# Kernel optimization log

Hardware: AMD Instinct MI355X
Metric: run time of the kernel (lower is better)

Reference implementation:

```python
import jax, jax.numpy as jnp
import numpy as np

N = 50000          # nodes
E = 1_600_000      # edges (avg degree 32)
IN_N, IN_E = 16, 1 # fc_encoder hardwired input dims
H = 128            # per-layer out_node/out_edge channels (out//2 = 64 inner)
BN_EPS = 1e-5


def setup_inputs() -> dict:
    key = jax.random.key(0)
    ks = jax.random.split(key, 32)
    d = {}
    d["x"] = jax.random.normal(ks[0], (N, IN_N), jnp.float32)
    d["edge_attr"] = jax.random.normal(ks[1], (E, IN_E), jnp.float32)
    d["edge_index"] = jax.random.randint(ks[2], (2, E), 0, N)
    i = 3
    for l, (ni, ei) in enumerate([(IN_N, IN_E), (H, H)]):
        s_n = 1.0 / np.sqrt(ni)
        s_e = 1.0 / np.sqrt(ei)
        s_h = 1.0 / np.sqrt(H)
        d[f"l{l}_Wn"] = jax.random.normal(ks[i], (H // 2, ni), jnp.float32) * s_n; i += 1
        d[f"l{l}_We"] = jax.random.normal(ks[i], (H // 2, ei), jnp.float32) * s_e; i += 1
        d[f"l{l}_Wfn"] = jax.random.normal(ks[i], (H, H), jnp.float32) * s_h; i += 1
        d[f"l{l}_bfn"] = jax.random.normal(ks[i], (H,), jnp.float32) * s_h; i += 1
        d[f"l{l}_Wfe"] = jax.random.normal(ks[i], (H, H), jnp.float32) * s_h; i += 1
        d[f"l{l}_bfe"] = jax.random.normal(ks[i], (H,), jnp.float32) * s_h; i += 1
        d[f"l{l}_g"] = jax.random.uniform(ks[i], (H,), jnp.float32, 0.5, 1.5); i += 1
        d[f"l{l}_b"] = jax.random.normal(ks[i], (H,), jnp.float32) * 0.1; i += 1
        d[f"l{l}_rm"] = jax.random.normal(ks[i], (H,), jnp.float32) * 0.1; i += 1
        d[f"l{l}_rv"] = jax.random.uniform(ks[i], (H,), jnp.float32, 0.5, 1.5); i += 1
    return d


def _layer(x, ea, src, dst, Wn, We, Wfn, bfn, Wfe, bfe, g, b, rm, rv):
    # NodeEdgeInteraction_node (eval mode: dropout = identity)
    n1 = jax.nn.relu(x @ Wn.T)            # [N, H/2]
    e1 = jax.nn.relu(ea @ We.T)           # [E, H/2]
    # edge_updater: cat([n1[src] + n1[dst], e1])
    e2 = jnp.concatenate([n1[src] + n1[dst], e1], axis=-1)      # [E, H]
    # propagate: message = e1, sum-aggregate at destination (edge_index[1])
    agg = jax.ops.segment_sum(e1, dst, num_segments=x.shape[0])  # [N, H/2]
    n2 = jnp.concatenate([agg, n1], axis=-1)                     # [N, H]
    n2 = jax.nn.relu(n2 @ Wfn.T + bfn)
    e2 = jax.nn.relu(e2 @ Wfe.T + bfe)
    # BatchNorm1d (eval: running stats)
    n2 = (n2 - rm) * jax.lax.rsqrt(rv + BN_EPS) * g + b
    return n2, e2


def reference(x, edge_attr, edge_index,
              l0_Wn, l0_We, l0_Wfn, l0_bfn, l0_Wfe, l0_bfe, l0_g, l0_b, l0_rm, l0_rv,
              l1_Wn, l1_We, l1_Wfn, l1_bfn, l1_Wfe, l1_bfe, l1_g, l1_b, l1_rm, l1_rv):
    src, dst = edge_index[0], edge_index[1]
    x, edge_attr = _layer(x, edge_attr, src, dst,
                          l0_Wn, l0_We, l0_Wfn, l0_bfn, l0_Wfe, l0_bfe,
                          l0_g, l0_b, l0_rm, l0_rv)
    x, edge_attr = _layer(x, edge_attr, src, dst,
                          l1_Wn, l1_We, l1_Wfn, l1_bfn, l1_Wfe, l1_bfe,
                          l1_g, l1_b, l1_rm, l1_rv)
    return x  # GNNEncoder returns node embeddings only
```

## Files before the change

kernel.cpp:

```cpp
#include <hip/hip_runtime.h>

typedef unsigned short u16;
typedef __attribute__((ext_vector_type(8))) short short8;
typedef __attribute__((ext_vector_type(4))) float floatx4;

#define NN 50000
#define NE 1600000
#define BN_EPS 1e-5f

__device__ __forceinline__ float bfu(u16 u) {
    union { unsigned u32; float f; } v; v.u32 = ((unsigned)u) << 16; return v.f;
}
__device__ __forceinline__ u16 f2bf(float f) {
    union { float f; unsigned u; } v; v.f = f;
    unsigned r = v.u + 0x7FFFu + ((v.u >> 16) & 1u);
    return (u16)(r >> 16);
}
__device__ __forceinline__ float ldf(const void* p, int i, int m) {
    return m ? ((const float*)p)[i] : bfu(((const u16*)p)[i]);
}

__global__ __launch_bounds__(256) void k_detect(const u16* __restrict__ x, int* __restrict__ mode) {
    float mx = 0.f;
    for (int i = threadIdx.x; i < 4096; i += 256) mx = fmaxf(mx, fabsf(bfu(x[i])));
#pragma unroll
    for (int o = 32; o > 0; o >>= 1) mx = fmaxf(mx, __shfl_down(mx, o));
    __shared__ float s[4];
    if ((threadIdx.x & 63) == 0) s[threadIdx.x >> 6] = mx;
    __syncthreads();
    if (threadIdx.x == 0) {
        float m2 = fmaxf(fmaxf(s[0], s[1]), fmaxf(s[2], s[3]));
        mode[0] = (m2 > 1e4f) ? 1 : 0;
    }
}

__global__ __launch_bounds__(256) void k_cvtw(const void* __restrict__ W0, const void* __restrict__ W1,
                                              const void* __restrict__ W2, const void* __restrict__ W3,
                                              const void* __restrict__ W4,
                                              u16* __restrict__ dst, const int* __restrict__ mf) {
    int m = mf[0];
    int i = blockIdx.x * 256 + threadIdx.x;
    const void* src; int off;
    if (i < 16384)      { src = W0; off = i; }
    else if (i < 24576) { src = W1; off = i - 16384; }
    else if (i < 40960) { src = W2; off = i - 24576; }
    else if (i < 49152) { src = W3; off = i - 40960; }
    else                { src = W4; off = i - 49152; }
    dst[i] = m ? f2bf(((const float*)src)[off]) : ((const u16*)src)[off];
}

__global__ __launch_bounds__(256) void k_enc0(const void* __restrict__ x, const void* __restrict__ Wn,
                                              u16* __restrict__ n1, const int* __restrict__ mf) {
    int m = mf[0];
    __shared__ float Wns[64 * 17];
    __shared__ float xsh[4][16];
    int t = threadIdx.x;
    int n0 = blockIdx.x * 4;
    for (int i = t; i < 1024; i += 256) Wns[(i >> 4) * 17 + (i & 15)] = ldf(Wn, i, m);
    if (t < 64) xsh[t >> 4][t & 15] = ldf(x, n0 * 16 + t, m);
    __syncthreads();
    int n = t >> 6, c = t & 63;
    float acc = 0.f;
#pragma unroll
    for (int i = 0; i < 16; i++) acc += xsh[n][i] * Wns[c * 17 + i];
    n1[(n0 + n) * 64 + c] = f2bf(fmaxf(acc, 0.f));
}

__global__ __launch_bounds__(256) void k_esum(const void* __restrict__ ea, const int* __restrict__ ei,
                                              float* __restrict__ sp, float* __restrict__ sn,
                                              const int* __restrict__ mf) {
    int m = mf[0];
    int e = blockIdx.x * 256 + threadIdx.x;
    float a = ldf(ea, e, m);
    int d = ei[NE + e];
    if (a > 0.f) atomicAdd(sp + d, a);
    else if (a < 0.f) atomicAdd(sn + d, a);
}

__global__ void k_pn(const void* __restrict__ We0, const void* __restrict__ Wfe0,
                     float* __restrict__ PN, const int* __restrict__ mf) {
    int m = mf[0];
    int j = threadIdx.x;
    float p = 0.f, n = 0.f;
    for (int k = 0; k < 64; k++) {
        float w = ldf(We0, k, m);
        float wf = ldf(Wfe0, j * 128 + 64 + k, m);
        p += fmaxf(w, 0.f) * wf;
        n += fminf(w, 0.f) * wf;
    }
    PN[j] = p; PN[128 + j] = n;
}

__global__ __launch_bounds__(256) void k_node_l0(
    const u16* __restrict__ n1l0, const float* __restrict__ sp, const float* __restrict__ sn,
    const void* __restrict__ We0, const u16* __restrict__ Wfn0c, const void* __restrict__ bfn0,
    const void* __restrict__ g0, const void* __restrict__ b0,
    const void* __restrict__ rm0, const void* __restrict__ rv0,
    const u16* __restrict__ Wn1c, u16* __restrict__ n1l1, const int* __restrict__ mf) {
    int m = mf[0];
    __shared__ __align__(16) u16 fs[64][136];
    __shared__ __align__(16) u16 xs[64][136];
    int t = threadIdx.x;
    int n0 = blockIdx.x * 64;
    {
        int col = t & 127;
        int rbase = t >> 7;
        float wp = 0.f, wn = 0.f;
        if (col < 64) { float w0 = ldf(We0, col, m); wp = fmaxf(w0, 0.f); wn = fminf(w0, 0.f); }
#pragma unroll
        for (int i = 0; i < 32; i++) {
            int row = rbase + 2 * i;
            int n = n0 + row;
            float v = 0.f;
            if (n < NN) v = (col < 64) ? (wp * sp[n] + wn * sn[n]) : bfu(n1l0[n * 64 + col - 64]);
            fs[row][col] = f2bf(v);
        }
    }
    __syncthreads();
    int lane = t & 63, w = t >> 6, q = lane >> 4, nidx = lane & 15;
    {
        const u16* ar = &fs[w * 16 + nidx][0];
        short8 a0 = *(const short8*)&ar[q * 8];
        short8 a1 = *(const short8*)&ar[32 + q * 8];
        short8 a2 = *(const short8*)&ar[64 + q * 8];
        short8 a3 = *(const short8*)&ar[96 + q * 8];
#pragma unroll
        for (int jt = 0; jt < 8; jt++) {
            int j = jt * 16 + nidx;
            const u16* wr = Wfn0c + j * 128;
            floatx4 acc = {0.f, 0.f, 0.f, 0.f};
            acc = __builtin_amdgcn_mfma_f32_16x16x32_bf16(a0, *(const short8*)&wr[q * 8], acc, 0, 0, 0);
            acc = __builtin_amdgcn_mfma_f32_16x16x32_bf16(a1, *(const short8*)&wr[32 + q * 8], acc, 0, 0, 0);
            acc = __builtin_amdgcn_mfma_f32_16x16x32_bf16(a2, *(const short8*)&wr[64 + q * 8], acc, 0, 0, 0);
            acc = __builtin_amdgcn_mfma_f32_16x16x32_bf16(a3, *(const short8*)&wr[96 + q * 8], acc, 0, 0, 0);
            float bias = ldf(bfn0, j, m);
            float sc = ldf(g0, j, m) * rsqrtf(ldf(rv0, j, m) + BN_EPS);
            float sh = ldf(b0, j, m) - ldf(rm0, j, m) * sc;
#pragma unroll
            for (int r = 0; r < 4; r++) {
                int row = w * 16 + q * 4 + r;
                xs[row][j] = f2bf(fmaxf(acc[r] + bias, 0.f) * sc + sh);
            }
        }
    }
    __syncthreads();
    {
        const u16* ar = &xs[w * 16 + nidx][0];
        short8 a0 = *(const short8*)&ar[q * 8];
        short8 a1 = *(const short8*)&ar[32 + q * 8];
        short8 a2 = *(const short8*)&ar[64 + q * 8];
        short8 a3 = *(const short8*)&ar[96 + q * 8];
#pragma unroll
        for (int jt = 0; jt < 4; jt++) {
            int j = jt * 16 + nidx;
            const u16* wr = Wn1c + j * 128;
            floatx4 acc = {0.f, 0.f, 0.f, 0.f};
            acc = __builtin_amdgcn_mfma_f32_16x16x32_bf16(a0, *(const short8*)&wr[q * 8], acc, 0, 0, 0);
            acc = __builtin_amdgcn_mfma_f32_16x16x32_bf16(a1, *(const short8*)&wr[32 + q * 8], acc, 0, 0, 0);
            acc = __builtin_amdgcn_mfma_f32_16x16x32_bf16(a2, *(const short8*)&wr[64 + q * 8], acc, 0, 0, 0);
            acc = __builtin_amdgcn_mfma_f32_16x16x32_bf16(a3, *(const short8*)&wr[96 + q * 8], acc, 0, 0, 0);
#pragma unroll
            for (int r = 0; r < 4; r++) {
                int row = w * 16 + q * 4 + r;
                int n = n0 + row;
                if (n < NN) n1l1[n * 64 + j] = f2bf(fmaxf(acc[r], 0.f));
            }
        }
    }
}

__global__ __launch_bounds__(256) void k_edge(
    const void* __restrict__ ea, const int* __restrict__ ei,
    const u16* __restrict__ n1l0,
    const u16* __restrict__ Wfe0c, const void* __restrict__ bfe0,
    const float* __restrict__ PN,
    const u16* __restrict__ We1c,
    float* __restrict__ agg, const int* __restrict__ mf) {
    int m = mf[0];
    __shared__ __align__(16) u16 h0s[16][72];
    __shared__ __align__(16) u16 h1s[16][136];
    __shared__ float aes[16];
    __shared__ int dsts[16];
    __shared__ int srcs[16];
    int t = threadIdx.x;
    int e0 = blockIdx.x * 16;
    if (t < 16) {
        int eg = e0 + t;
        aes[t] = ldf(ea, eg, m);
        srcs[t] = ei[eg];
        dsts[t] = ei[NE + eg];
    }
    __syncthreads();
#pragma unroll
    for (int i = 0; i < 4; i++) {
        int idx = t + i * 256;
        int e = idx >> 6, c = idx & 63;
        float v = bfu(n1l0[srcs[e] * 64 + c]) + bfu(n1l0[dsts[e] * 64 + c]);
        h0s[e][c] = f2bf(v);
    }
    __syncthreads();
    int lane = t & 63;
    int w = t >> 6;
    int q = lane >> 4;
    int nidx = lane & 15;
    short8 a0 = *(const short8*)&h0s[nidx][q * 8];
    short8 a1 = *(const short8*)&h0s[nidx][32 + q * 8];
#pragma unroll
    for (int jj = 0; jj < 2; jj++) {
        int jt = 2 * w + jj;
        int j = jt * 16 + nidx;
        const u16* wrow = Wfe0c + j * 128;
        short8 b0 = *(const short8*)&wrow[q * 8];
        short8 b1 = *(const short8*)&wrow[32 + q * 8];
        floatx4 acc = {0.f, 0.f, 0.f, 0.f};
        acc = __builtin_amdgcn_mfma_f32_16x16x32_bf16(a0, b0, acc, 0, 0, 0);
        acc = __builtin_amdgcn_mfma_f32_16x16x32_bf16(a1, b1, acc, 0, 0, 0);
        float bias = ldf(bfe0, j, m);
        float Pj = PN[j], Nj = PN[128 + j];
#pragma unroll
        for (int r = 0; r < 4; r++) {
            int e = q * 4 + r;
            float a = aes[e];
            float v = acc[r] + bias + a * (a > 0.f ? Pj : Nj);
            h1s[e][j] = f2bf(fmaxf(v, 0.f));
        }
    }
    __syncthreads();
    {
        int c = w * 16 + nidx;
        const u16* wrow = We1c + c * 128;
        floatx4 acc = {0.f, 0.f, 0.f, 0.f};
#pragma unroll
        for (int ks = 0; ks < 4; ks++) {
            short8 aa = *(const short8*)&h1s[nidx][ks * 32 + q * 8];
            short8 bb = *(const short8*)&wrow[ks * 32 + q * 8];
            acc = __builtin_amdgcn_mfma_f32_16x16x32_bf16(aa, bb, acc, 0, 0, 0);
        }
#pragma unroll
        for (int r = 0; r < 4; r++) {
            int e = q * 4 + r;
            float v = fmaxf(acc[r], 0.f);
            atomicAdd(agg + dsts[e] * 64 + c, v);
        }
    }
}

__global__ __launch_bounds__(256) void k_node_l1(
    const u16* __restrict__ n1l1, const float* __restrict__ agg,
    const u16* __restrict__ Wfn1c, const void* __restrict__ bfn1,
    const void* __restrict__ g1, const void* __restrict__ b1,
    const void* __restrict__ rm1, const void* __restrict__ rv1,
    void* __restrict__ out, const int* __restrict__ mf) {
    int m = mf[0];
    __shared__ __align__(16) u16 fs[64][136];
    int t = threadIdx.x;
    int n0 = blockIdx.x * 64;
    {
        int col = t & 127;
        int rbase = t >> 7;
#pragma unroll
        for (int i = 0; i < 32; i++) {
            int row = rbase + 2 * i;
            int n = n0 + row;
            float v = 0.f;
            if (n < NN) v = (col < 64) ? agg[n * 64 + col] : bfu(n1l1[n * 64 + col - 64]);
            fs[row][col] = f2bf(v);
        }
    }
    __syncthreads();
    int lane = t & 63, w = t >> 6, q = lane >> 4, nidx = lane & 15;
    const u16* ar = &fs[w * 16 + nidx][0];
    short8 a0 = *(const short8*)&ar[q * 8];
    short8 a1 = *(const short8*)&ar[32 + q * 8];
    short8 a2 = *(const short8*)&ar[64 + q * 8];
    short8 a3 = *(const short8*)&ar[96 + q * 8];
#pragma unroll
    for (int jt = 0; jt < 8; jt++) {
        int j = jt * 16 + nidx;
        const u16* wr = Wfn1c + j * 128;
        floatx4 acc = {0.f, 0.f, 0.f, 0.f};
        acc = __builtin_amdgcn_mfma_f32_16x16x32_bf16(a0, *(const short8*)&wr[q * 8], acc, 0, 0, 0);
        acc = __builtin_amdgcn_mfma_f32_16x16x32_bf16(a1, *(const short8*)&wr[32 + q * 8], acc, 0, 0, 0);
        acc = __builtin_amdgcn_mfma_f32_16x16x32_bf16(a2, *(const short8*)&wr[64 + q * 8], acc, 0, 0, 0);
        acc = __builtin_amdgcn_mfma_f32_16x16x32_bf16(a3, *(const short8*)&wr[96 + q * 8], acc, 0, 0, 0);
        float bias = ldf(bfn1, j, m);
        float sc = ldf(g1, j, m) * rsqrtf(ldf(rv1, j, m) + BN_EPS);
        float sh = ldf(b1, j, m) - ldf(rm1, j, m) * sc;
#pragma unroll
        for (int r = 0; r < 4; r++) {
            int row = w * 16 + q * 4 + r;
            int n = n0 + row;
            if (n < NN) {
                float v = fmaxf(acc[r] + bias, 0.f) * sc + sh;
                if (m) ((float*)out)[n * 128 + j] = v;
                else   ((u16*)out)[n * 128 + j] = f2bf(v);
            }
        }
    }
}

extern "C" void kernel_launch(void* const* d_in, const int* in_sizes, int n_in,
                              void* d_out, int out_size, void* d_ws, size_t ws_size,
                              hipStream_t stream) {
    const void* x    = d_in[0];
    const void* ea   = d_in[1];
    const int*  ei   = (const int*)d_in[2];
    const void* Wn0  = d_in[3];
    const void* We0  = d_in[4];
    const void* Wfn0 = d_in[5];
    const void* bfn0 = d_in[6];
    const void* Wfe0 = d_in[7];
    const void* bfe0 = d_in[8];
    const void* g0   = d_in[9];
    const void* b0   = d_in[10];
    const void* rm0  = d_in[11];
    const void* rv0  = d_in[12];
    const void* Wn1  = d_in[13];
    const void* We1  = d_in[14];
    const void* Wfn1 = d_in[15];
    const void* bfn1 = d_in[16];
    const void* g1   = d_in[19];
    const void* b1   = d_in[20];
    const void* rm1  = d_in[21];
    const void* rv1  = d_in[22];

    float* wsf   = (float*)d_ws;
    float* agg   = wsf;
    u16*   n1l0  = (u16*)(wsf + 3200000);
    u16*   n1l1  = (u16*)(wsf + 4800000);
    float* sp    = wsf + 6400000;
    float* sn    = wsf + 6450000;
    float* PN    = wsf + 6500000;
    u16*   Wc    = (u16*)(wsf + 6500256);
    int*   mode  = (int*)(wsf + 6533024);
    u16* Wfe0c = Wc;
    u16* We1c  = Wc + 16384;
    u16* Wfn0c = Wc + 24576;
    u16* Wn1c  = Wc + 40960;
    u16* Wfn1c = Wc + 49152;

    hipMemsetAsync(sp, 0, 100000 * sizeof(float), stream);
    hipMemsetAsync(agg, 0, 3200000 * sizeof(float), stream);

    k_detect<<<1, 256, 0, stream>>>((const u16*)x, mode);
    k_cvtw<<<256, 256, 0, stream>>>(Wfe0, We1, Wfn0, Wn1, Wfn1, Wc, mode);
    k_enc0<<<12500, 256, 0, stream>>>(x, Wn0, n1l0, mode);
    k_esum<<<6250, 256, 0, stream>>>(ea, ei, sp, sn, mode);
    k_pn<<<1, 128, 0, stream>>>(We0, Wfe0, PN, mode);
    k_node_l0<<<782, 256, 0, stream>>>(n1l0, sp, sn, We0, Wfn0c, bfn0,
                                       g0, b0, rm0, rv0, Wn1c, n1l1, mode);
    k_edge<<<100000, 256, 0, stream>>>(ea, ei, n1l0, Wfe0c, bfe0, PN, We1c, agg, mode);
    k_node_l1<<<782, 256, 0, stream>>>(n1l1, agg, Wfn1c, bfn1,
                                       g1, b1, rm1, rv1, d_out, mode);
}
```

Before: 713.6 us.

## Sort edges by destination (CSR) and aggregate per-node in shared memory

Builds a destination-sorted CSR by counting in-degree, running a three-kernel prefix scan, and scattering the source index plus edge attribute into permuted arrays. The edge kernel then handles blocks of 8 destination nodes: it caches their n1 rows in shared memory and accumulates messages with shared-memory atomics, so the 1.6M×64 global atomicAdds and the agg memset go away. The cost is extra scan and scatter passes with global atomics, and partially filled 16-edge tiles. The packing into perm assumes source indices fit in 16 bits, which fails for N=50000 (src up to 49999 > 65535? no, fits), though block work is now imbalanced across nodes of differing degree.

After: 1.129 ms. 58.2% more time.

```diff
diff --git a/kernel.cpp b/kernel.cpp
--- a/kernel.cpp
+++ b/kernel.cpp
@@ -7,6 +7,8 @@
 #define NN 50000
 #define NE 1600000
 #define BN_EPS 1e-5f
+#define NPB 8
+#define NSCAN 196
 
 __device__ __forceinline__ float bfu(u16 u) {
     union { unsigned u32; float f; } v; v.u32 = ((unsigned)u) << 16; return v.f;
@@ -68,13 +70,72 @@
 
 __global__ __launch_bounds__(256) void k_esum(const void* __restrict__ ea, const int* __restrict__ ei,
                                               float* __restrict__ sp, float* __restrict__ sn,
-                                              const int* __restrict__ mf) {
+                                              int* __restrict__ cnt, const int* __restrict__ mf) {
     int m = mf[0];
     int e = blockIdx.x * 256 + threadIdx.x;
     float a = ldf(ea, e, m);
     int d = ei[NE + e];
+    atomicAdd(cnt + d, 1);
     if (a > 0.f) atomicAdd(sp + d, a);
     else if (a < 0.f) atomicAdd(sn + d, a);
+}
+
+__global__ __launch_bounds__(256) void k_scan1(const int* __restrict__ cnt, int* __restrict__ bsum) {
+    int t = threadIdx.x;
+    int idx = blockIdx.x * 256 + t;
+    int v = (idx < NN) ? cnt[idx] : 0;
+#pragma unroll
+    for (int o = 32; o > 0; o >>= 1) v += __shfl_down(v, o);
+    __shared__ int s[4];
+    if ((t & 63) == 0) s[t >> 6] = v;
+    __syncthreads();
+    if (t == 0) bsum[blockIdx.x] = s[0] + s[1] + s[2] + s[3];
+}
+
+__global__ __launch_bounds__(256) void k_scan2(int* __restrict__ bsum) {
+    __shared__ int sh[256];
+    int t = threadIdx.x;
+    int v = (t < NSCAN) ? bsum[t] : 0;
+    sh[t] = v;
+    __syncthreads();
+    for (int o = 1; o < 256; o <<= 1) {
+        int u = (t >= o) ? sh[t - o] : 0;
+        __syncthreads();
+        sh[t] += u;
+        __syncthreads();
+    }
+    if (t < NSCAN) bsum[t] = sh[t] - v;
+}
+
+__global__ __launch_bounds__(256) void k_scan3(const int* __restrict__ cnt, const int* __restrict__ bsum,
+                                               int* __restrict__ start, int* __restrict__ cursor) {
+    __shared__ int sh[256];
+    int t = threadIdx.x;
+    int idx = blockIdx.x * 256 + t;
+    int v = (idx < NN) ? cnt[idx] : 0;
+    sh[t] = v;
+    __syncthreads();
+    for (int o = 1; o < 256; o <<= 1) {
+        int u = (t >= o) ? sh[t - o] : 0;
+        __syncthreads();
+        sh[t] += u;
+        __syncthreads();
+    }
+    int excl = sh[t] - v + bsum[blockIdx.x];
+    if (idx < NN) { start[idx] = excl; cursor[idx] = excl; }
+    if (idx == NN - 1) start[NN] = excl + v;
+}
+
+__global__ __launch_bounds__(256) void k_scatter(const void* __restrict__ ea, const int* __restrict__ ei,
+                                                 int* __restrict__ cursor, int* __restrict__ perm,
+                                                 float* __restrict__ eas, const int* __restrict__ mf) {
+    int m = mf[0];
+    int e = blockIdx.x * 256 + threadIdx.x;
+    int d = ei[NE + e];
+    int s = ei[e];
+    int p = atomicAdd(cursor + d, 1);
+    perm[p] = s | ((d & 7) << 16);
+    eas[p] = ldf(ea, e, m);
 }
 
 __global__ void k_pn(const void* __restrict__ We0, const void* __restrict__ Wfe0,
@@ -169,8 +230,8 @@
     }
 }
 
-__global__ __launch_bounds__(256) void k_edge(
-    const void* __restrict__ ea, const int* __restrict__ ei,
+__global__ __launch_bounds__(256) void k_edge2(
+    const float* __restrict__ eas, const int* __restrict__ perm, const int* __restrict__ startp,
     const u16* __restrict__ n1l0,
     const u16* __restrict__ Wfe0c, const void* __restrict__ bfe0,
     const float* __restrict__ PN,
@@ -179,69 +240,104 @@
     int m = mf[0];
     __shared__ __align__(16) u16 h0s[16][72];
     __shared__ __align__(16) u16 h1s[16][136];
+    __shared__ float dstv[NPB][64];
+    __shared__ float accs[NPB][64];
     __shared__ float aes[16];
-    __shared__ int dsts[16];
     __shared__ int srcs[16];
-    int t = threadIdx.x;
-    int e0 = blockIdx.x * 16;
-    if (t < 16) {
-        int eg = e0 + t;
-        aes[t] = ldf(ea, eg, m);
-        srcs[t] = ei[eg];
-        dsts[t] = ei[NE + eg];
-    }
-    __syncthreads();
-#pragma unroll
-    for (int i = 0; i < 4; i++) {
-        int idx = t + i * 256;
-        int e = idx >> 6, c = idx & 63;
-        float v = bfu(n1l0[srcs[e] * 64 + c]) + bfu(n1l0[dsts[e] * 64 + c]);
-        h0s[e][c] = f2bf(v);
-    }
-    __syncthreads();
-    int lane = t & 63;
-    int w = t >> 6;
-    int q = lane >> 4;
-    int nidx = lane & 15;
-    short8 a0 = *(const short8*)&h0s[nidx][q * 8];
-    short8 a1 = *(const short8*)&h0s[nidx][32 + q * 8];
-#pragma unroll
-    for (int jj = 0; jj < 2; jj++) {
-        int jt = 2 * w + jj;
-        int j = jt * 16 + nidx;
-        const u16* wrow = Wfe0c + j * 128;
-        short8 b0 = *(const short8*)&wrow[q * 8];
-        short8 b1 = *(const short8*)&wrow[32 + q * 8];
-        floatx4 acc = {0.f, 0.f, 0.f, 0.f};
-        acc = __builtin_amdgcn_mfma_f32_16x16x32_bf16(a0, b0, acc, 0, 0, 0);
-        acc = __builtin_amdgcn_mfma_f32_16x16x32_bf16(a1, b1, acc, 0, 0, 0);
-        float bias = ldf(bfe0, j, m);
-        float Pj = PN[j], Nj = PN[128 + j];
-#pragma unroll
-        for (int r = 0; r < 4; r++) {
-            int e = q * 4 + r;
-            float a = aes[e];
-            float v = acc[r] + bias + a * (a > 0.f ? Pj : Nj);
-            h1s[e][j] = f2bf(fmaxf(v, 0.f));
-        }
-    }
-    __syncthreads();
-    {
-        int c = w * 16 + nidx;
-        const u16* wrow = We1c + c * 128;
-        floatx4 acc = {0.f, 0.f, 0.f, 0.f};
-#pragma unroll
-        for (int ks = 0; ks < 4; ks++) {
-            short8 aa = *(const short8*)&h1s[nidx][ks * 32 + q * 8];
-            short8 bb = *(const short8*)&wrow[ks * 32 + q * 8];
-            acc = __builtin_amdgcn_mfma_f32_16x16x32_bf16(aa, bb, acc, 0, 0, 0);
-        }
-#pragma unroll
-        for (int r = 0; r < 4; r++) {
-            int e = q * 4 + r;
-            float v = fmaxf(acc[r], 0.f);
-            atomicAdd(agg + dsts[e] * 64 + c, v);
-        }
+    __shared__ int lids[16];
+    int t = threadIdx.x;
+    int n0 = blockIdx.x * NPB;
+    int s0 = startp[n0], s1 = startp[n0 + NPB];
+    for (int i = t; i < NPB * 64; i += 256) {
+        int lid = i >> 6, c = i & 63;
+        dstv[lid][c] = bfu(n1l0[(n0 + lid) * 64 + c]);
+        accs[lid][c] = 0.f;
+    }
+    int lane = t & 63, w = t >> 6, q = lane >> 4, nidx = lane & 15;
+    int j0 = (2 * w) * 16 + nidx, j1 = (2 * w + 1) * 16 + nidx;
+    const u16* wr0 = Wfe0c + j0 * 128;
+    const u16* wr1 = Wfe0c + j1 * 128;
+    short8 w0a = *(const short8*)&wr0[q * 8];
+    short8 w0b = *(const short8*)&wr0[32 + q * 8];
+    short8 w1a = *(const short8*)&wr1[q * 8];
+    short8 w1b = *(const short8*)&wr1[32 + q * 8];
+    float bias0 = ldf(bfe0, j0, m), bias1 = ldf(bfe0, j1, m);
+    float P0 = PN[j0], N0 = PN[128 + j0];
+    float P1 = PN[j1], N1 = PN[128 + j1];
+    int c2 = w * 16 + nidx;
+    const u16* wr2 = We1c + c2 * 128;
+    short8 w2_0 = *(const short8*)&wr2[q * 8];
+    short8 w2_1 = *(const short8*)&wr2[32 + q * 8];
+    short8 w2_2 = *(const short8*)&wr2[64 + q * 8];
+    short8 w2_3 = *(const short8*)&wr2[96 + q * 8];
+    __syncthreads();
+
+    for (int cb = s0; cb < s1; cb += 16) {
+        if (t < 16) {
+            int gi = cb + t;
+            int valid = gi < s1;
+            int v = valid ? perm[gi] : 0;
+            srcs[t] = v & 0xFFFF;
+            lids[t] = valid ? ((v >> 16) & 7) : -1;
+            aes[t] = valid ? eas[gi] : 0.f;
+        }
+        __syncthreads();
+#pragma unroll
+        for (int i = 0; i < 4; i++) {
+            int idx = t + i * 256;
+            int e = idx >> 6, c = idx & 63;
+            int lid = lids[e];
+            float v = bfu(n1l0[srcs[e] * 64 + c]) + (lid >= 0 ? dstv[lid][c] : 0.f);
+            h0s[e][c] = f2bf(v);
+        }
+        __syncthreads();
+        {
+            short8 a0 = *(const short8*)&h0s[nidx][q * 8];
+            short8 a1 = *(const short8*)&h0s[nidx][32 + q * 8];
+            {
+                floatx4 acc = {0.f, 0.f, 0.f, 0.f};
+                acc = __builtin_amdgcn_mfma_f32_16x16x32_bf16(a0, w0a, acc, 0, 0, 0);
+                acc = __builtin_amdgcn_mfma_f32_16x16x32_bf16(a1, w0b, acc, 0, 0, 0);
+#pragma unroll
+                for (int r = 0; r < 4; r++) {
+                    int e = q * 4 + r;
+                    float a = aes[e];
+                    float v = acc[r] + bias0 + a * (a > 0.f ? P0 : N0);
+                    h1s[e][j0] = f2bf(fmaxf(v, 0.f));
+                }
+            }
+            {
+                floatx4 acc = {0.f, 0.f, 0.f, 0.f};
+                acc = __builtin_amdgcn_mfma_f32_16x16x32_bf16(a0, w1a, acc, 0, 0, 0);
+                acc = __builtin_amdgcn_mfma_f32_16x16x32_bf16(a1, w1b, acc, 0, 0, 0);
+#pragma unroll
+                for (int r = 0; r < 4; r++) {
+                    int e = q * 4 + r;
+                    float a = aes[e];
+                    float v = acc[r] + bias1 + a * (a > 0.f ? P1 : N1);
+                    h1s[e][j1] = f2bf(fmaxf(v, 0.f));
+                }
+            }
+        }
+        __syncthreads();
+        {
+            floatx4 acc = {0.f, 0.f, 0.f, 0.f};
+            acc = __builtin_amdgcn_mfma_f32_16x16x32_bf16(*(const short8*)&h1s[nidx][q * 8],       w2_0, acc, 0, 0, 0);
+            acc = __builtin_amdgcn_mfma_f32_16x16x32_bf16(*(const short8*)&h1s[nidx][32 + q * 8],  w2_1, acc, 0, 0, 0);
+            acc = __builtin_amdgcn_mfma_f32_16x16x32_bf16(*(const short8*)&h1s[nidx][64 + q * 8],  w2_2, acc, 0, 0, 0);
+            acc = __builtin_amdgcn_mfma_f32_16x16x32_bf16(*(const short8*)&h1s[nidx][96 + q * 8],  w2_3, acc, 0, 0, 0);
+#pragma unroll
+            for (int r = 0; r < 4; r++) {
+                int e = q * 4 + r;
+                int lid = lids[e];
+                if (lid >= 0) atomicAdd(&accs[lid][c2], fmaxf(acc[r], 0.f));
+            }
+        }
+        __syncthreads();
+    }
+    for (int i = t; i < NPB * 64; i += 256) {
+        int lid = i >> 6, c = i & 63;
+        agg[(n0 + lid) * 64 + c] = accs[lid][c];
     }
 }
 
@@ -324,32 +420,42 @@
     const void* rm1  = d_in[21];
     const void* rv1  = d_in[22];
 
-    float* wsf   = (float*)d_ws;
-    float* agg   = wsf;
-    u16*   n1l0  = (u16*)(wsf + 3200000);
-    u16*   n1l1  = (u16*)(wsf + 4800000);
-    float* sp    = wsf + 6400000;
-    float* sn    = wsf + 6450000;
-    float* PN    = wsf + 6500000;
-    u16*   Wc    = (u16*)(wsf + 6500256);
-    int*   mode  = (int*)(wsf + 6533024);
+    float* wsf    = (float*)d_ws;
+    float* agg    = wsf;
+    u16*   n1l0   = (u16*)(wsf + 3200000);
+    u16*   n1l1   = (u16*)(wsf + 4800000);
+    float* sp     = wsf + 6400000;
+    float* sn     = wsf + 6450000;
+    int*   cnt    = (int*)(wsf + 6500000);
+    int*   start  = (int*)(wsf + 6550000);
+    int*   cursor = (int*)(wsf + 6600004);
+    int*   bsum   = (int*)(wsf + 6650004);
+    float* PN     = wsf + 6650260;
+    u16*   Wc     = (u16*)(wsf + 6650516);
+    int*   mode   = (int*)(wsf + 6683284);
+    int*   perm   = (int*)(wsf + 6683288);
+    float* eas    = wsf + 8283288;
     u16* Wfe0c = Wc;
     u16* We1c  = Wc + 16384;
     u16* Wfn0c = Wc + 24576;
     u16* Wn1c  = Wc + 40960;
     u16* Wfn1c = Wc + 49152;
 
-    hipMemsetAsync(sp, 0, 100000 * sizeof(float), stream);
-    hipMemsetAsync(agg, 0, 3200000 * sizeof(float), stream);
+    hipMemsetAsync(sp, 0, 150000 * sizeof(float), stream);
 
     k_detect<<<1, 256, 0, stream>>>((const u16*)x, mode);
     k_cvtw<<<256, 256, 0, stream>>>(Wfe0, We1, Wfn0, Wn1, Wfn1, Wc, mode);
     k_enc0<<<12500, 256, 0, stream>>>(x, Wn0, n1l0, mode);
-    k_esum<<<6250, 256, 0, stream>>>(ea, ei, sp, sn, mode);
+    k_esum<<<6250, 256, 0, stream>>>(ea, ei, sp, sn, cnt, mode);
+    k_scan1<<<NSCAN, 256, 0, stream>>>(cnt, bsum);
+    k_scan2<<<1, 256, 0, stream>>>(bsum);
+    k_scan3<<<NSCAN, 256, 0, stream>>>(cnt, bsum, start, cursor);
     k_pn<<<1, 128, 0, stream>>>(We0, Wfe0, PN, mode);
+    k_scatter<<<6250, 256, 0, stream>>>(ea, ei, cursor, perm, eas, mode);
     k_node_l0<<<782, 256, 0, stream>>>(n1l0, sp, sn, We0, Wfn0c, bfn0,
                                        g0, b0, rm0, rv0, Wn1c, n1l1, mode);
-    k_edge<<<100000, 256, 0, stream>>>(ea, ei, n1l0, Wfe0c, bfe0, PN, We1c, agg, mode);
+    k_edge2<<<NN / NPB, 256, 0, stream>>>(eas, perm, start, n1l0, Wfe0c, bfe0,
+                                          PN, We1c, agg, mode);
     k_node_l1<<<782, 256, 0, stream>>>(n1l1, agg, Wfn1c, bfn1,
                                        g1, b1, rm1, rv1, d_out, mode);
 }
```

## Counting-sort edges by destination and pre-reduce scatter-adds per segment

Applied to the files above, without the earlier changes.

Edges are bucketed by destination node with a counting sort (degree count, three-pass scan, atomic-cursor scatter) into a packed src/dst/attr array. The edge kernel then reads these sorted records. Within each 16-edge tile it sums the layer-1 edge messages per destination segment in shared memory, then issues one global atomic per segment and channel instead of one per edge and channel. This targets the roughly hundred million global float atomics into the aggregation buffer and improves dst locality. The cost is extra scan and scatter kernels, a nondeterministic edge order, and a packing scheme that relies on node ids fitting in 16 bits.

Result: slower. 904.6 us (+26.8%).

```diff
diff --git a/kernel.cpp b/kernel.cpp
--- a/kernel.cpp
+++ b/kernel.cpp
@@ -7,6 +7,7 @@
 #define NN 50000
 #define NE 1600000
 #define BN_EPS 1e-5f
+#define NSCAN 196
 
 __device__ __forceinline__ float bfu(u16 u) {
     union { unsigned u32; float f; } v; v.u32 = ((unsigned)u) << 16; return v.f;
@@ -68,13 +69,74 @@
 
 __global__ __launch_bounds__(256) void k_esum(const void* __restrict__ ea, const int* __restrict__ ei,
                                               float* __restrict__ sp, float* __restrict__ sn,
-                                              const int* __restrict__ mf) {
+                                              int* __restrict__ cnt, const int* __restrict__ mf) {
     int m = mf[0];
     int e = blockIdx.x * 256 + threadIdx.x;
     float a = ldf(ea, e, m);
     int d = ei[NE + e];
+    atomicAdd(cnt + d, 1);
     if (a > 0.f) atomicAdd(sp + d, a);
     else if (a < 0.f) atomicAdd(sn + d, a);
+}
+
+__global__ __launch_bounds__(256) void k_scan1(const int* __restrict__ cnt, int* __restrict__ bsum) {
+    int t = threadIdx.x;
+    int idx = blockIdx.x * 256 + t;
+    int v = (idx < NN) ? cnt[idx] : 0;
+#pragma unroll
+    for (int o = 32; o > 0; o >>= 1) v += __shfl_down(v, o);
+    __shared__ int s[4];
+    if ((t & 63) == 0) s[t >> 6] = v;
+    __syncthreads();
+    if (t == 0) bsum[blockIdx.x] = s[0] + s[1] + s[2] + s[3];
+}
+
+__global__ __launch_bounds__(256) void k_scan2(int* __restrict__ bsum) {
+    __shared__ int sh[256];
+    int t = threadIdx.x;
+    int v = (t < NSCAN) ? bsum[t] : 0;
+    sh[t] = v;
+    __syncthreads();
+    for (int o = 1; o < 256; o <<= 1) {
+        int u = (t >= o) ? sh[t - o] : 0;
+        __syncthreads();
+        sh[t] += u;
+        __syncthreads();
+    }
+    if (t < NSCAN) bsum[t] = sh[t] - v;
+}
+
+__global__ __launch_bounds__(256) void k_scan3(const int* __restrict__ cnt, const int* __restrict__ bsum,
+                                               int* __restrict__ cursor) {
+    __shared__ int sh[256];
+    int t = threadIdx.x;
+    int idx = blockIdx.x * 256 + t;
+    int v = (idx < NN) ? cnt[idx] : 0;
+    sh[t] = v;
+    __syncthreads();
+    for (int o = 1; o < 256; o <<= 1) {
+        int u = (t >= o) ? sh[t - o] : 0;
+        __syncthreads();
+        sh[t] += u;
+        __syncthreads();
+    }
+    int excl = sh[t] - v + bsum[blockIdx.x];
+    if (idx < NN) cursor[idx] = excl;
+}
+
+__global__ __launch_bounds__(256) void k_scatter(const void* __restrict__ ea, const int* __restrict__ ei,
+                                                 int* __restrict__ cursor, int2* __restrict__ edata,
+                                                 const int* __restrict__ mf) {
+    int m = mf[0];
+    int e = blockIdx.x * 256 + threadIdx.x;
+    int d = ei[NE + e];
+    int s = ei[e];
+    float a = ldf(ea, e, m);
+    int p = atomicAdd(cursor + d, 1);
+    int2 v;
+    v.x = (int)((unsigned)s | ((unsigned)d << 16));
+    v.y = __float_as_int(a);
+    edata[p] = v;
 }
 
 __global__ void k_pn(const void* __restrict__ We0, const void* __restrict__ Wfe0,
@@ -169,66 +231,72 @@
     }
 }
 
-__global__ __launch_bounds__(256) void k_edge(
-    const void* __restrict__ ea, const int* __restrict__ ei,
-    const u16* __restrict__ n1l0,
+__global__ __launch_bounds__(256) void k_edge3(
+    const int2* __restrict__ edata, const u16* __restrict__ n1l0,
     const u16* __restrict__ Wfe0c, const void* __restrict__ bfe0,
-    const float* __restrict__ PN,
-    const u16* __restrict__ We1c,
+    const float* __restrict__ PN, const u16* __restrict__ We1c,
     float* __restrict__ agg, const int* __restrict__ mf) {
     int m = mf[0];
     __shared__ __align__(16) u16 h0s[16][72];
     __shared__ __align__(16) u16 h1s[16][136];
+    __shared__ float hacc[16][68];
     __shared__ float aes[16];
     __shared__ int dsts[16];
-    __shared__ int srcs[16];
+    __shared__ int segs[16];
     int t = threadIdx.x;
     int e0 = blockIdx.x * 16;
+    int2 ed = edata[e0 + (t & 15)];
     if (t < 16) {
-        int eg = e0 + t;
-        aes[t] = ldf(ea, eg, m);
-        srcs[t] = ei[eg];
-        dsts[t] = ei[NE + eg];
-    }
-    __syncthreads();
+        dsts[t] = (int)(((unsigned)ed.x) >> 16);
+        aes[t] = __int_as_float(ed.y);
+    }
+    for (int i = t; i < 16 * 68; i += 256) ((float*)hacc)[i] = 0.f;
+    if (t < 16) {
+        int s = t;
+        while (s > 0 && dsts[s - 1] == dsts[s]) s--;
+        segs[t] = s;
+    }
+    int lane = t & 63, w = t >> 6;
 #pragma unroll
     for (int i = 0; i < 4; i++) {
         int idx = t + i * 256;
         int e = idx >> 6, c = idx & 63;
-        float v = bfu(n1l0[srcs[e] * 64 + c]) + bfu(n1l0[dsts[e] * 64 + c]);
+        unsigned me = (unsigned)__shfl(ed.x, e);
+        int srcn = (int)(me & 0xFFFFu);
+        int dstn = (int)(me >> 16);
+        float v = bfu(n1l0[srcn * 64 + c]) + bfu(n1l0[dstn * 64 + c]);
         h0s[e][c] = f2bf(v);
     }
     __syncthreads();
-    int lane = t & 63;
-    int w = t >> 6;
-    int q = lane >> 4;
-    int nidx = lane & 15;
-    short8 a0 = *(const short8*)&h0s[nidx][q * 8];
-    short8 a1 = *(const short8*)&h0s[nidx][32 + q * 8];
-#pragma unroll
-    for (int jj = 0; jj < 2; jj++) {
-        int jt = 2 * w + jj;
-        int j = jt * 16 + nidx;
-        const u16* wrow = Wfe0c + j * 128;
-        short8 b0 = *(const short8*)&wrow[q * 8];
-        short8 b1 = *(const short8*)&wrow[32 + q * 8];
-        floatx4 acc = {0.f, 0.f, 0.f, 0.f};
-        acc = __builtin_amdgcn_mfma_f32_16x16x32_bf16(a0, b0, acc, 0, 0, 0);
-        acc = __builtin_amdgcn_mfma_f32_16x16x32_bf16(a1, b1, acc, 0, 0, 0);
-        float bias = ldf(bfe0, j, m);
-        float Pj = PN[j], Nj = PN[128 + j];
-#pragma unroll
-        for (int r = 0; r < 4; r++) {
-            int e = q * 4 + r;
-            float a = aes[e];
-            float v = acc[r] + bias + a * (a > 0.f ? Pj : Nj);
-            h1s[e][j] = f2bf(fmaxf(v, 0.f));
-        }
-    }
-    __syncthreads();
-    {
-        int c = w * 16 + nidx;
-        const u16* wrow = We1c + c * 128;
+    int q = lane >> 4, nidx = lane & 15;
+    {
+        short8 a0 = *(const short8*)&h0s[nidx][q * 8];
+        short8 a1 = *(const short8*)&h0s[nidx][32 + q * 8];
+#pragma unroll
+        for (int jj = 0; jj < 2; jj++) {
+            int jt = 2 * w + jj;
+            int j = jt * 16 + nidx;
+            const u16* wrow = Wfe0c + j * 128;
+            short8 b0 = *(const short8*)&wrow[q * 8];
+            short8 b1 = *(const short8*)&wrow[32 + q * 8];
+            floatx4 acc = {0.f, 0.f, 0.f, 0.f};
+            acc = __builtin_amdgcn_mfma_f32_16x16x32_bf16(a0, b0, acc, 0, 0, 0);
+            acc = __builtin_amdgcn_mfma_f32_16x16x32_bf16(a1, b1, acc, 0, 0, 0);
+            float bias = ldf(bfe0, j, m);
+            float Pj = PN[j], Nj = PN[128 + j];
+#pragma unroll
+            for (int r = 0; r < 4; r++) {
+                int e = q * 4 + r;
+                float a = aes[e];
+                float v = acc[r] + bias + a * (a > 0.f ? Pj : Nj);
+                h1s[e][j] = f2bf(fmaxf(v, 0.f));
+            }
+        }
+    }
+    __syncthreads();
+    {
+        int c2 = w * 16 + nidx;
+        const u16* wrow = We1c + c2 * 128;
         floatx4 acc = {0.f, 0.f, 0.f, 0.f};
 #pragma unroll
         for (int ks = 0; ks < 4; ks++) {
@@ -236,12 +304,26 @@
             short8 bb = *(const short8*)&wrow[ks * 32 + q * 8];
             acc = __builtin_amdgcn_mfma_f32_16x16x32_bf16(aa, bb, acc, 0, 0, 0);
         }
-#pragma unroll
-        for (int r = 0; r < 4; r++) {
-            int e = q * 4 + r;
+        int eb = q * 4;
+        float run = fmaxf(acc[0], 0.f);
+        int cur = segs[eb];
+#pragma unroll
+        for (int r = 1; r < 4; r++) {
+            int sg = segs[eb + r];
             float v = fmaxf(acc[r], 0.f);
-            atomicAdd(agg + dsts[e] * 64 + c, v);
-        }
+            if (sg != cur) {
+                atomicAdd(&hacc[cur][c2], run);
+                run = v; cur = sg;
+            } else {
+                run += v;
+            }
+        }
+        atomicAdd(&hacc[cur][c2], run);
+    }
+    __syncthreads();
+    for (int i = t; i < 1024; i += 256) {
+        int e = i >> 6, c = i & 63;
+        if (segs[e] == e) atomicAdd(agg + dsts[e] * 64 + c, hacc[e][c]);
     }
 }
 
@@ -324,32 +406,40 @@
     const void* rm1  = d_in[21];
     const void* rv1  = d_in[22];
 
-    float* wsf   = (float*)d_ws;
-    float* agg   = wsf;
-    u16*   n1l0  = (u16*)(wsf + 3200000);
-    u16*   n1l1  = (u16*)(wsf + 4800000);
-    float* sp    = wsf + 6400000;
-    float* sn    = wsf + 6450000;
-    float* PN    = wsf + 6500000;
-    u16*   Wc    = (u16*)(wsf + 6500256);
-    int*   mode  = (int*)(wsf + 6533024);
+    float* wsf    = (float*)d_ws;
+    float* agg    = wsf;
+    u16*   n1l0   = (u16*)(wsf + 3200000);
+    u16*   n1l1   = (u16*)(wsf + 4800000);
+    float* sp     = wsf + 6400000;
+    float* sn     = wsf + 6450000;
+    int*   cnt    = (int*)(wsf + 6500000);
+    int*   cursor = (int*)(wsf + 6600004);
+    int*   bsum   = (int*)(wsf + 6650004);
+    float* PN     = wsf + 6650260;
+    u16*   Wc     = (u16*)(wsf + 6650516);
+    int*   mode   = (int*)(wsf + 6683284);
+    int2*  edata  = (int2*)(wsf + 6683288);
     u16* Wfe0c = Wc;
     u16* We1c  = Wc + 16384;
     u16* Wfn0c = Wc + 24576;
     u16* Wn1c  = Wc + 40960;
     u16* Wfn1c = Wc + 49152;
 
-    hipMemsetAsync(sp, 0, 100000 * sizeof(float), stream);
+    hipMemsetAsync(sp, 0, 150000 * sizeof(float), stream);
     hipMemsetAsync(agg, 0, 3200000 * sizeof(float), stream);
 
     k_detect<<<1, 256, 0, stream>>>((const u16*)x, mode);
     k_cvtw<<<256, 256, 0, stream>>>(Wfe0, We1, Wfn0, Wn1, Wfn1, Wc, mode);
     k_enc0<<<12500, 256, 0, stream>>>(x, Wn0, n1l0, mode);
-    k_esum<<<6250, 256, 0, stream>>>(ea, ei, sp, sn, mode);
+    k_esum<<<6250, 256, 0, stream>>>(ea, ei, sp, sn, cnt, mode);
+    k_scan1<<<NSCAN, 256, 0, stream>>>(cnt, bsum);
+    k_scan2<<<1, 256, 0, stream>>>(bsum);
+    k_scan3<<<NSCAN, 256, 0, stream>>>(cnt, bsum, cursor);
     k_pn<<<1, 128, 0, stream>>>(We0, Wfe0, PN, mode);
+    k_scatter<<<6250, 256, 0, stream>>>(ea, ei, cursor, edata, mode);
     k_node_l0<<<782, 256, 0, stream>>>(n1l0, sp, sn, We0, Wfn0c, bfn0,
                                        g0, b0, rm0, rv0, Wn1c, n1l1, mode);
-    k_edge<<<100000, 256, 0, stream>>>(ea, ei, n1l0, Wfe0c, bfe0, PN, We1c, agg, mode);
+    k_edge3<<<NE / 16, 256, 0, stream>>>(edata, n1l0, Wfe0c, bfe0, PN, We1c, agg, mode);
     k_node_l1<<<782, 256, 0, stream>>>(n1l1, agg, Wfn1c, bfn1,
                                        g1, b1, rm1, rv1, d_out, mode);
 }
```
